# Kernel optimization log

Hardware: AMD Instinct MI355X
Metric: run time of the kernel (lower is better)

## Reference

```python
import jax, jax.numpy as jnp
import numpy as np

B, L, D, H, V = 4, 2048, 512, 8, 50257
NCAND, K, MAXM, NL, DFF = 64, 5, 10, 2, 4 * 512
HD = D // H


def _ln(x, g, b, eps=1e-5):
    m = jnp.mean(x, -1, keepdims=True)
    v = jnp.mean((x - m) ** 2, -1, keepdims=True)
    return (x - m) * jax.lax.rsqrt(v + eps) * g + b


def _mha(x, in_w, in_b, out_w, out_b):
    Bx, Lx, Dx = x.shape
    qkv = x @ in_w.T + in_b                      # [B,L,3D]
    q, k, v = jnp.split(qkv, 3, axis=-1)
    heads = lambda t: t.reshape(Bx, Lx, H, HD).transpose(0, 2, 1, 3)  # [B,H,L,hd]
    q, k, v = heads(q), heads(k), heads(v)
    s = jnp.einsum('bhqd,bhkd->bhqk', q, k) * np.float32(1.0 / np.sqrt(HD))
    a = jax.nn.softmax(s, axis=-1)
    o = jnp.einsum('bhqk,bhkd->bhqd', a, v).transpose(0, 2, 1, 3).reshape(Bx, Lx, Dx)
    return o @ out_w.T + out_b


def _encoder(x, p):
    # torch TransformerEncoderLayer default: post-LN, ReLU, dropout off (eval)
    for i in range(NL):
        x = _ln(x + _mha(x, p['attn_in_w'][i], p['attn_in_b'][i], p['attn_out_w'][i], p['attn_out_b'][i]), p['ln1_g'][i], p['ln1_b'][i])
        h = jax.nn.relu(x @ p['ffn_w1'][i].T + p['ffn_b1'][i]) @ p['ffn_w2'][i].T + p['ffn_b2'][i]
        x = _ln(x + h, p['ln2_g'][i], p['ln2_b'][i])
    return x


def _forward(token_ids, candidate_embeds, p):
    x = p['tok_emb'][token_ids] + p['pos_emb'][jnp.arange(L)][None]
    hidden = _encoder(x, p)                                  # [B,L,D]
    start_logits = hidden @ p['start_w'] + p['start_b']      # [B,L]
    end_logits = hidden @ p['end_w'] + p['end_b']
    s_idx = jax.lax.top_k(start_logits, K)[1]                # [B,K]
    e_idx = jax.lax.top_k(end_logits, K)[1]
    valid = (e_idx >= s_idx) & ((e_idx - s_idx) < MAXM)      # span validity mask
    h_s = jnp.take_along_axis(hidden, s_idx[..., None], axis=1)  # [B,K,D]
    h_e = jnp.take_along_axis(hidden, e_idx[..., None], axis=1)
    feat = jnp.concatenate([h_s, h_e, h_s * h_e], axis=-1)   # [B,K,3D]
    span = jax.nn.relu(feat @ p['span_w1'].T + p['span_b1']) @ p['span_w2'].T + p['span_b2']
    # compact valid spans to the front (ragged-to-padded), pad rest with zeros
    order = jnp.argsort((~valid).astype(jnp.int32), axis=1)  # stable: valid first
    span = jnp.take_along_axis(span, order[..., None], axis=1)
    vs = jnp.take_along_axis(valid, order, axis=1)
    span = span * vs[..., None].astype(span.dtype)           # [B,K,D]
    mp = span @ p['mention_w'].T + p['mention_b']
    cp = candidate_embeds @ p['entity_w'].T + p['entity_b']
    scores = jnp.einsum('bmd,bmcd->bmc', mp, cp)             # [B,K,NCAND]
    return span, start_logits, end_logits, hidden, scores


PARAM_KEYS = ['tok_emb', 'pos_emb', 'attn_in_w', 'attn_in_b', 'attn_out_w', 'attn_out_b',
              'ln1_g', 'ln1_b', 'ffn_w1', 'ffn_b1', 'ffn_w2', 'ffn_b2', 'ln2_g', 'ln2_b',
              'start_w', 'start_b', 'end_w', 'end_b', 'span_w1', 'span_b1', 'span_w2', 'span_b2',
              'mention_w', 'mention_b', 'entity_w', 'entity_b']


def setup_inputs() -> dict:
    key = jax.random.key(0)
    ks = iter(jax.random.split(key, 32))
    n = lambda shape, s=0.02: jax.random.normal(next(ks), shape, jnp.float32) * s
    return {
        'token_ids': jax.random.randint(next(ks), (B, L), 0, V),
        'candidate_embeds': jax.random.normal(next(ks), (B, K, NCAND, D), jnp.float32),
        'tok_emb': n((V, D)), 'pos_emb': n((L, D)),
        'attn_in_w': n((NL, 3 * D, D)), 'attn_in_b': n((NL, 3 * D)),
        'attn_out_w': n((NL, D, D)), 'attn_out_b': n((NL, D)),
        'ln1_g': jnp.ones((NL, D)), 'ln1_b': jnp.zeros((NL, D)),
        'ffn_w1': n((NL, DFF, D)), 'ffn_b1': n((NL, DFF)),
        'ffn_w2': n((NL, D, DFF)), 'ffn_b2': n((NL, D)),
        'ln2_g': jnp.ones((NL, D)), 'ln2_b': jnp.zeros((NL, D)),
        'start_w': n((D,)), 'start_b': jnp.zeros(()),
        'end_w': n((D,)), 'end_b': jnp.zeros(()),
        'span_w1': n((D, 3 * D)), 'span_b1': jnp.zeros((D,)),
        'span_w2': n((D, D)), 'span_b2': jnp.zeros((D,)),
        'mention_w': n((D, D)), 'mention_b': jnp.zeros((D,)),
        'entity_w': n((D, D)), 'entity_b': jnp.zeros((D,)),
    }


def reference(token_ids, candidate_embeds, tok_emb, pos_emb, attn_in_w, attn_in_b, attn_out_w, attn_out_b,
              ln1_g, ln1_b, ffn_w1, ffn_b1, ffn_w2, ffn_b2, ln2_g, ln2_b,
              start_w, start_b, end_w, end_b, span_w1, span_b1, span_w2, span_b2,
              mention_w, mention_b, entity_w, entity_b):
    loc = locals()
    p = {k: loc[k] for k in PARAM_KEYS}
    return _forward(token_ids, candidate_embeds, p)
```

## Files before the change

### kernel.cpp

```cpp
#include <hip/hip_runtime.h>
#include <hip/hip_bf16.h>
#include <cstddef>

#define BQ 4
#define LQ 2048
#define DQ 512
#define HQ 8
#define HDQ 64
#define KQ 5
#define MAXMQ 10

typedef __attribute__((ext_vector_type(8))) __bf16 bf16x8;
typedef __attribute__((ext_vector_type(4))) __bf16 bf16x4;
typedef __attribute__((ext_vector_type(4))) float f32x4;

__device__ inline void gload_lds16(const void* g, void* l) {
  __builtin_amdgcn_global_load_lds(
      (const __attribute__((address_space(1))) unsigned*)g,
      (__attribute__((address_space(3))) unsigned*)l, 16, 0, 0);
}

__device__ inline unsigned pack_bf16(float a, float b) {
  unsigned short ua = __builtin_bit_cast(unsigned short, (__bf16)a);
  unsigned short ub = __builtin_bit_cast(unsigned short, (__bf16)b);
  return (unsigned)ua | ((unsigned)ub << 16);
}

__device__ inline unsigned pack2(__bf16 a, __bf16 b) {
  return (unsigned)__builtin_bit_cast(unsigned short, a) |
         ((unsigned)__builtin_bit_cast(unsigned short, b) << 16);
}

__device__ inline float bf_lo(unsigned u) {
  return (float)__builtin_bit_cast(__bf16, (unsigned short)(u & 0xffff));
}
__device__ inline float bf_hi(unsigned u) {
  return (float)__builtin_bit_cast(__bf16, (unsigned short)(u >> 16));
}

__global__ __launch_bounds__(256) void prep_kernel(
    const float* __restrict__ s0, const float* __restrict__ s1,
    const float* __restrict__ s2, const float* __restrict__ s3,
    __bf16* __restrict__ d0, __bf16* __restrict__ d1,
    __bf16* __restrict__ d2, __bf16* __restrict__ d3,
    const float* __restrict__ ew_in, float* __restrict__ ew_out,
    const int* __restrict__ tok, const float* __restrict__ te,
    const float* __restrict__ pe, __bf16* __restrict__ xb) {
  __shared__ float t[32][33];
  const int bid = blockIdx.x;
  if (bid < 3072) {
    size_t g = ((size_t)bid * 256 + threadIdx.x) * 8;
    const float* src; __bf16* dst; size_t e;
    if (g < 1572864)      { src = s0; dst = d0; e = g; }
    else if (g < 2097152) { src = s1; dst = d1; e = g - 1572864; }
    else if (g < 4194304) { src = s2; dst = d2; e = g - 2097152; }
    else                  { src = s3; dst = d3; e = g - 4194304; }
    float4 a = *(const float4*)(src + e);
    float4 b = *(const float4*)(src + e + 4);
    bf16x8 v;
    v[0] = (__bf16)a.x; v[1] = (__bf16)a.y; v[2] = (__bf16)a.z; v[3] = (__bf16)a.w;
    v[4] = (__bf16)b.x; v[5] = (__bf16)b.y; v[6] = (__bf16)b.z; v[7] = (__bf16)b.w;
    *(bf16x8*)(dst + e) = v;
  } else if (bid < 3328) {
    int blk = bid - 3072;
    int bx = blk & 15, by = blk >> 4;
    int cx = threadIdx.x & 31, ry = threadIdx.x >> 5;
    #pragma unroll
    for (int i = 0; i < 4; ++i)
      t[ry + i * 8][cx] = ew_in[(size_t)(by * 32 + ry + i * 8) * 512 + bx * 32 + cx];
    __syncthreads();
    #pragma unroll
    for (int i = 0; i < 4; ++i)
      ew_out[(size_t)(bx * 32 + ry + i * 8) * 512 + by * 32 + cx] = t[cx][ry + i * 8];
  } else {
    int row = bid - 3328;
    int l = row & (LQ - 1);
    int tk = tok[row];
    int d = 2 * threadIdx.x;
    float2 tv = *(const float2*)&te[(size_t)tk * DQ + d];
    float2 pv = *(const float2*)&pe[(size_t)l * DQ + d];
    *(unsigned*)&xb[(size_t)row * DQ + d] = pack_bf16(tv.x + pv.x, tv.y + pv.y);
  }
}

template<int BN, bool RELU, bool HASRES>
__global__ __launch_bounds__(256) void bgemm_kernel(
    const __bf16* __restrict__ A, const __bf16* __restrict__ W,
    const float* __restrict__ bias, const __bf16* __restrict__ R,
    __bf16* __restrict__ Cb, int M, int N, int K) {
  __shared__ __bf16 As[2][128][32];
  __shared__ __bf16 Bs[2][BN][32];
  constexpr int NF = BN / 32;
  const int tid = threadIdx.x;
  const int w = tid >> 6, lane = tid & 63;
  const int lr = lane & 15, lg = lane >> 4;
  const int wr = w >> 1, wc = w & 1;
  const int m0 = blockIdx.y * 128, n0 = blockIdx.x * BN;

  f32x4 acc[4][NF];
  #pragma unroll
  for (int m = 0; m < 4; ++m)
    #pragma unroll
    for (int n = 0; n < NF; ++n) acc[m][n] = f32x4{0.f, 0.f, 0.f, 0.f};

  const int srowA = w * 32 + (lane >> 2);
  const int scol = (lane & 3) * 8;
  const int srowB = (BN == 128) ? srowA : (w * 16 + (lane >> 2));
  const __bf16* Ag = A + (size_t)(m0 + srowA) * K + scol;
  const __bf16* Bg = W + (size_t)(n0 + srowB) * K + scol;

  const int NT = K / 32;

  auto stage = [&](int t, int buf) {
    const int k1 = t * 32;
    gload_lds16(Ag + k1, &As[buf][w * 32][0]);
    gload_lds16(Ag + 16 * K + k1, &As[buf][w * 32 + 16][0]);
    if (BN == 128) {
      gload_lds16(Bg + k1, &Bs[buf][(w * 32) % BN][0]);
      gload_lds16(Bg + 16 * K + k1, &Bs[buf][(w * 32 + 16) % BN][0]);
    } else {
      gload_lds16(Bg + k1, &Bs[buf][(w * 16) % BN][0]);
    }
  };

  auto step = [&](int t, int cur) {
    __syncthreads();
    if (t + 1 < NT) stage(t + 1, cur ^ 1);
    bf16x8 af[4], bfr[NF];
    #pragma unroll
    for (int m = 0; m < 4; ++m) af[m] = *(bf16x8*)&As[cur][wr * 64 + m * 16 + lr][lg * 8];
    #pragma unroll
    for (int n = 0; n < NF; ++n) bfr[n] = *(bf16x8*)&Bs[cur][wc * (BN / 2) + n * 16 + lr][lg * 8];
    __builtin_amdgcn_s_setprio(1);
    #pragma unroll
    for (int m = 0; m < 4; ++m)
      #pragma unroll
      for (int n = 0; n < NF; ++n)
        acc[m][n] = __builtin_amdgcn_mfma_f32_16x16x32_bf16(af[m], bfr[n], acc[m][n], 0, 0, 0);
    __builtin_amdgcn_s_setprio(0);
  };

  stage(0, 0);
  for (int t = 0; t < NT; t += 2) { step(t, 0); step(t + 1, 1); }

  const int crow = m0 + wr * 64 + lg * 4;
  const int ccol = n0 + wc * (BN / 2) + lr;
  #pragma unroll
  for (int n = 0; n < NF; ++n) {
    int gc = ccol + n * 16;
    float bn = bias ? bias[gc] : 0.f;
    #pragma unroll
    for (int m = 0; m < 4; ++m) {
      #pragma unroll
      for (int reg = 0; reg < 4; ++reg) {
        int gr = crow + m * 16 + reg;
        float v = acc[m][n][reg] + bn;
        if (HASRES) v += (float)R[(size_t)gr * N + gc];
        if (RELU) v = fmaxf(v, 0.f);
        Cb[(size_t)gr * N + gc] = (__bf16)v;
      }
    }
  }
}

template<int MR, bool RELU, bool MASK>
__global__ __launch_bounds__(256) void tinygemm_kernel(
    const float* __restrict__ A, const float* __restrict__ W,
    const float* __restrict__ bias, const int* __restrict__ vs,
    float* __restrict__ C, int N, int K) {
  int n = blockIdx.x * 4 + (threadIdx.x >> 6);
  int lane = threadIdx.x & 63;
  if (n >= N) return;
  const float* wr = W + (size_t)n * K;
  float acc[MR];
  #pragma unroll
  for (int m = 0; m < MR; ++m) acc[m] = 0.f;
  for (int k = lane; k < K; k += 64) {
    float wv = wr[k];
    #pragma unroll
    for (int m = 0; m < MR; ++m)
      acc[m] += A[(size_t)m * K + k] * wv;
  }
  #pragma unroll
  for (int m = 0; m < MR; ++m) {
    #pragma unroll
    for (int off = 32; off; off >>= 1) acc[m] += __shfl_xor(acc[m], off);
  }
  if (lane == 0) {
    float bn = bias ? bias[n] : 0.f;
    #pragma unroll
    for (int m = 0; m < MR; ++m) {
      float v = acc[m] + bn;
      if (RELU) v = fmaxf(v, 0.f);
      if (MASK) v *= (float)vs[m];
      C[(size_t)m * N + n] = v;
    }
  }
}

__global__ __launch_bounds__(512) void attn_mfma_kernel(const __bf16* __restrict__ qkv,
                                                        __bf16* __restrict__ ob) {
  __shared__ __bf16 Ks[2][4096];
  __shared__ __bf16 Vt[2][64][72];
  __shared__ __bf16 Ps[8][1024];

  const int tid = threadIdx.x;
  const int wave = tid >> 6;
  const int lane = tid & 63;
  const int lr = lane & 15;
  const int lg = lane >> 4;

  const int bid = blockIdx.x;
  const int swz = (bid & 7) * 64 + (bid >> 3);
  const int bh = swz >> 4;
  const int qb = swz & 15;
  const int b = bh >> 3, h = bh & 7;
  const int q0 = qb * 128 + wave * 16;

  const __bf16* base = qkv + (size_t)b * LQ * 1536;

  bf16x8 aq[2];
  {
    const __bf16* qp = base + (size_t)(q0 + lr) * 1536 + h * 64 + lg * 8;
    aq[0] = *(const bf16x8*)qp;
    aq[1] = *(const bf16x8*)(qp + 32);
  }

  const int krow = tid >> 3;
  const int kdc = (tid & 7) ^ (krow & 7);
  const __bf16* gK = base + (size_t)krow * 1536 + 512 + h * 64 + kdc * 8;

  const int pr2 = tid >> 4;
  const int dq = tid & 15;
  const int vd0 = dq * 4;
  const __bf16* gV = base + (size_t)(2 * pr2) * 1536 + 1024 + h * 64 + vd0;
  const int pc2 = 2 * (pr2 & 3) + 8 * ((pr2 >> 2) ^ (dq >> 1));

  const int STEP = 64 * 1536;

  float lsum = 0.f;
  f32x4 o_acc[4];
  #pragma unroll
  for (int df = 0; df < 4; ++df) o_acc[df] = f32x4{0.f, 0.f, 0.f, 0.f};

  const float KE = 0.125f * 1.44269504f;

  gload_lds16(gK, &Ks[0][64 * wave * 8]);
  {
    bf16x4 v0 = *(const bf16x4*)gV;
    bf16x4 v1 = *(const bf16x4*)(gV + 1536);
    #pragma unroll
    for (int i = 0; i < 4; ++i)
      *(unsigned*)&Vt[0][vd0 + i][pc2] = pack2(v0[i], v1[i]);
  }
  gK += STEP; gV += STEP;

  auto tile = [&](int cur, bool more) {
    __syncthreads();
    bf16x4 nv0, nv1;
    if (more) {
      gload_lds16(gK, &Ks[cur ^ 1][64 * wave * 8]);
      nv0 = *(const bf16x4*)gV;
      nv1 = *(const bf16x4*)(gV + 1536);
      gK += STEP; gV += STEP;
    }

    f32x4 s[4];
    __builtin_amdgcn_s_setprio(1);
    #pragma unroll
    for (int f = 0; f < 4; ++f) {
      f32x4 acc = f32x4{0.f, 0.f, 0.f, 0.f};
      #pragma unroll
      for (int c = 0; c < 2; ++c) {
        bf16x8 ak = *(bf16x8*)&Ks[cur][(f * 16 + lr) * 64 + (((4 * c + lg) ^ (lr & 7)) << 3)];
        acc = __builtin_amdgcn_mfma_f32_16x16x32_bf16(ak, aq[c], acc, 0, 0, 0);
      }
      s[f] = acc;
    }
    __builtin_amdgcn_s_setprio(0);

    float rs = 0.f;
    #pragma unroll
    for (int f = 0; f < 4; ++f)
      #pragma unroll
      for (int r = 0; r < 4; ++r) {
        float p = exp2f(s[f][r] * KE);
        s[f][r] = p;
        rs += p;
      }
    rs += __shfl_xor(rs, 16);
    rs += __shfl_xor(rs, 32);
    lsum += rs;

    #pragma unroll
    for (int f = 0; f < 4; ++f) {
      uint2 pv;
      pv.x = pack_bf16(s[f][0], s[f][1]);
      pv.y = pack_bf16(s[f][2], s[f][3]);
      int chunk = 2 * f + (lg >> 1);
      int eoff = ((chunk ^ (lr & 7)) << 3) + ((lg & 1) << 2);
      *(uint2*)&Ps[wave][lr * 64 + eoff] = pv;
    }

    #pragma unroll
    for (int kc = 0; kc < 2; ++kc) {
      bf16x8 bp = *(bf16x8*)&Ps[wave][lr * 64 + (((4 * kc + lg) ^ (lr & 7)) << 3)];
      __builtin_amdgcn_s_setprio(1);
      #pragma unroll
      for (int df = 0; df < 4; ++df) {
        int vrow = df * 16 + lr;
        int pb = (((4 * kc + lg) ^ ((vrow >> 3) & 7)) << 3);
        bf16x8 av = *(bf16x8*)&Vt[cur][vrow][pb];
        o_acc[df] = __builtin_amdgcn_mfma_f32_16x16x32_bf16(av, bp, o_acc[df], 0, 0, 0);
      }
      __builtin_amdgcn_s_setprio(0);
    }

    if (more) {
      #pragma unroll
      for (int i = 0; i < 4; ++i)
        *(unsigned*)&Vt[cur ^ 1][vd0 + i][pc2] = pack2(nv0[i], nv1[i]);
    }
  };

  for (int kt = 0; kt < LQ / 64; kt += 2) {
    tile(0, true);
    tile(1, kt + 1 != LQ / 64 - 1);
  }

  float inv = 1.f / lsum;
  __bf16* orow = ob + ((size_t)(b * LQ) + q0 + lr) * DQ + h * 64 + lg * 4;
  #pragma unroll
  for (int df = 0; df < 4; ++df) {
    uint2 ov;
    ov.x = pack_bf16(o_acc[df][0] * inv, o_acc[df][1] * inv);
    ov.y = pack_bf16(o_acc[df][2] * inv, o_acc[df][3] * inv);
    *(uint2*)(orow + df * 16) = ov;
  }
}

template<bool WF32>
__global__ __launch_bounds__(256) void ln_kernel(const __bf16* __restrict__ t,
    const float* __restrict__ g, const float* __restrict__ bb,
    __bf16* __restrict__ xb, float* __restrict__ xf) {
  int row = blockIdx.x;
  int tid = threadIdx.x;
  unsigned u = *(const unsigned*)&t[(size_t)row * DQ + 2 * tid];
  float v0 = bf_lo(u), v1 = bf_hi(u);
  float s = v0 + v1, ss = v0 * v0 + v1 * v1;
  #pragma unroll
  for (int off = 32; off; off >>= 1) { s += __shfl_xor(s, off); ss += __shfl_xor(ss, off); }
  __shared__ float rs[4], rss[4];
  int w = tid >> 6;
  if ((tid & 63) == 0) { rs[w] = s; rss[w] = ss; }
  __syncthreads();
  s = rs[0] + rs[1] + rs[2] + rs[3];
  ss = rss[0] + rss[1] + rss[2] + rss[3];
  float mean = s * (1.f / 512.f);
  float var = ss * (1.f / 512.f) - mean * mean;
  float r = rsqrtf(var + 1e-5f);
  float2 gg = *(const float2*)&g[2 * tid];
  float2 bv = *(const float2*)&bb[2 * tid];
  float o0 = (v0 - mean) * r * gg.x + bv.x;
  float o1 = (v1 - mean) * r * gg.y + bv.y;
  *(unsigned*)&xb[(size_t)row * DQ + 2 * tid] = pack_bf16(o0, o1);
  if (WF32) {
    float2 of; of.x = o0; of.y = o1;
    *(float2*)&xf[(size_t)row * DQ + 2 * tid] = of;
  }
}

__global__ __launch_bounds__(256) void logits_kernel(const float* __restrict__ hidden,
    const float* __restrict__ sw, const float* __restrict__ sb,
    const float* __restrict__ ew, const float* __restrict__ eb,
    float* __restrict__ osl, float* __restrict__ oel) {
  int row = blockIdx.x * 4 + (threadIdx.x >> 6);
  int lane = threadIdx.x & 63;
  const float* hr = hidden + (size_t)row * DQ;
  float a = 0.f, b2 = 0.f;
  #pragma unroll
  for (int i = 0; i < 8; ++i) {
    int d = lane + i * 64;
    float h = hr[d];
    a += h * sw[d];
    b2 += h * ew[d];
  }
  #pragma unroll
  for (int off = 32; off; off >>= 1) { a += __shfl_xor(a, off); b2 += __shfl_xor(b2, off); }
  if (lane == 0) { osl[row] = a + sb[0]; oel[row] = b2 + eb[0]; }
}

__global__ void topk_kernel(const float* __restrict__ slog, const float* __restrict__ elog,
                            int* __restrict__ sidx, int* __restrict__ eidx) {
  int b = blockIdx.x & 3;
  int which = blockIdx.x >> 2;
  const float* lg = (which ? elog : slog) + (size_t)b * LQ;
  int* outp = (which ? eidx : sidx) + b * KQ;
  int lane = threadIdx.x;
  int ch[KQ];
  for (int k = 0; k < KQ; ++k) {
    float bv = -1e38f; int bi = 1 << 30;
    for (int i = lane; i < LQ; i += 64) {
      bool skip = false;
      for (int t = 0; t < k; ++t) if (ch[t] == i) skip = true;
      float v = lg[i];
      if (!skip && (v > bv || (v == bv && i < bi))) { bv = v; bi = i; }
    }
    #pragma unroll
    for (int off = 32; off; off >>= 1) {
      float ov = __shfl_xor(bv, off); int oi = __shfl_xor(bi, off);
      if (ov > bv || (ov == bv && oi < bi)) { bv = ov; bi = oi; }
    }
    ch[k] = bi;
    if (lane == 0) outp[k] = bi;
  }
}

__global__ void vo_kernel(const int* __restrict__ sidx, const int* __restrict__ eidx,
                          int* __restrict__ order, int* __restrict__ vs) {
  int b = threadIdx.x;
  if (b >= BQ) return;
  int val[KQ];
  for (int k = 0; k < KQ; ++k) {
    int s = sidx[b * KQ + k], e = eidx[b * KQ + k];
    val[k] = (e >= s && (e - s) < MAXMQ) ? 1 : 0;
  }
  int j = 0;
  for (int k = 0; k < KQ; ++k) if (val[k])  { order[b * KQ + j] = k; vs[b * KQ + j] = 1; ++j; }
  for (int k = 0; k < KQ; ++k) if (!val[k]) { order[b * KQ + j] = k; vs[b * KQ + j] = 0; ++j; }
}

__global__ __launch_bounds__(256) void feat_kernel(const float* __restrict__ hidden,
    const int* __restrict__ sidx, const int* __restrict__ eidx,
    const int* __restrict__ order, float* __restrict__ feat) {
  int row = blockIdx.x;
  int b = row / KQ;
  int k = order[row];
  int si = sidx[b * KQ + k], ei = eidx[b * KQ + k];
  const float* hs = hidden + ((size_t)(b * LQ + si)) * DQ;
  const float* he = hidden + ((size_t)(b * LQ + ei)) * DQ;
  float* fr = feat + (size_t)row * (3 * DQ);
  for (int d = threadIdx.x; d < DQ; d += 256) {
    float a = hs[d], c = he[d];
    fr[d] = a; fr[DQ + d] = c; fr[2 * DQ + d] = a * c;
  }
}

__global__ __launch_bounds__(256) void scores_kernel(const float* __restrict__ cand,
    const float* __restrict__ mp, const float* __restrict__ u, const float* __restrict__ ebias,
    float* __restrict__ oscores) {
  int gw = blockIdx.x * 4 + (threadIdx.x >> 6);
  int lane = threadIdx.x & 63;
  int bj = gw >> 6;
  const float* ce = cand + (size_t)gw * DQ;
  const float* ur = u + (size_t)bj * DQ;
  const float* mr = mp + (size_t)bj * DQ;
  float s = 0.f;
  #pragma unroll
  for (int i = 0; i < 8; ++i) {
    int e = lane + i * 64;
    s += ce[e] * ur[e] + mr[e] * ebias[e];
  }
  #pragma unroll
  for (int off = 32; off; off >>= 1) s += __shfl_xor(s, off);
  if (lane == 0) oscores[gw] = s;
}

extern "C" void kernel_launch(void* const* d_in, const int* in_sizes, int n_in,
                              void* d_out, int out_size, void* d_ws, size_t ws_size,
                              hipStream_t stream) {
  const int*   token_ids = (const int*)d_in[0];
  const float* cand    = (const float*)d_in[1];
  const float* tok_emb = (const float*)d_in[2];
  const float* pos_emb = (const float*)d_in[3];
  const float* ain_w   = (const float*)d_in[4];
  const float* ain_b   = (const float*)d_in[5];
  const float* aout_w  = (const float*)d_in[6];
  const float* aout_b  = (const float*)d_in[7];
  const float* ln1g    = (const float*)d_in[8];
  const float* ln1b    = (const float*)d_in[9];
  const float* fw1     = (const float*)d_in[10];
  const float* fb1     = (const float*)d_in[11];
  const float* fw2     = (const float*)d_in[12];
  const float* fb2     = (const float*)d_in[13];
  const float* ln2g    = (const float*)d_in[14];
  const float* ln2b    = (const float*)d_in[15];
  const float* sw      = (const float*)d_in[16];
  const float* sb      = (const float*)d_in[17];
  const float* ew      = (const float*)d_in[18];
  const float* eb      = (const float*)d_in[19];
  const float* sp_w1   = (const float*)d_in[20];
  const float* sp_b1   = (const float*)d_in[21];
  const float* sp_w2   = (const float*)d_in[22];
  const float* sp_b2   = (const float*)d_in[23];
  const float* m_w     = (const float*)d_in[24];
  const float* m_b     = (const float*)d_in[25];
  const float* e_w     = (const float*)d_in[26];
  const float* e_b     = (const float*)d_in[27];

  const int M = BQ * LQ;
  float* out = (float*)d_out;
  float* out_span   = out;
  float* out_sl     = out + 10240;
  float* out_el     = out + 18432;
  float* out_hidden = out + 26624;
  float* out_scores = out + 4220928;

  float* ws  = (float*)d_ws;
  __bf16* BIGb = (__bf16*)ws;
  __bf16* Xb   = (__bf16*)(ws + 8388608);
  __bf16* Ob   = (__bf16*)(ws + 10485760);
  __bf16* Tb   = (__bf16*)(ws + 12582912);
  __bf16* ain_wb  = (__bf16*)(ws + 14680064);
  __bf16* aout_wb = (__bf16*)(ws + 15466496);
  __bf16* fw1b    = (__bf16*)(ws + 15728640);
  __bf16* fw2b    = (__bf16*)(ws + 16777216);
  float* e_wT     = ws + 17825792;
  int*   SIDX  = (int*)(ws + 18088064);
  int*   EIDX  = SIDX + 20;
  int*   ORDER = EIDX + 20;
  int*   VS    = ORDER + 20;
  float* FEAT    = ws + 18088192;
  float* SPANH   = FEAT + 30720;
  float* MP      = SPANH + 10240;
  float* U       = MP + 10240;

  prep_kernel<<<11520, 256, 0, stream>>>(ain_w, aout_w, fw1, fw2,
                                         ain_wb, aout_wb, fw1b, fw2b,
                                         e_w, e_wT, token_ids, tok_emb, pos_emb, Xb);

  for (int l = 0; l < 2; ++l) {
    bgemm_kernel<128, false, false><<<dim3(12, 64), 256, 0, stream>>>(
        Xb, ain_wb + (size_t)l * 1536 * 512, ain_b + l * 1536, nullptr,
        BIGb, M, 1536, 512);
    attn_mfma_kernel<<<512, 512, 0, stream>>>(BIGb, Ob);
    bgemm_kernel<128, false, true><<<dim3(4, 64), 256, 0, stream>>>(
        Ob, aout_wb + (size_t)l * 512 * 512, aout_b + l * 512, Xb,
        Tb, M, 512, 512);
    ln_kernel<false><<<M, 256, 0, stream>>>(Tb, ln1g + l * 512, ln1b + l * 512,
                                            Xb, nullptr);
    bgemm_kernel<128, true, false><<<dim3(16, 64), 256, 0, stream>>>(
        Xb, fw1b + (size_t)l * 2048 * 512, fb1 + l * 2048, nullptr,
        BIGb, M, 2048, 512);
    bgemm_kernel<128, false, true><<<dim3(4, 64), 256, 0, stream>>>(
        BIGb, fw2b + (size_t)l * 512 * 2048, fb2 + l * 512, Xb,
        Tb, M, 512, 2048);
    if (l == 0)
      ln_kernel<false><<<M, 256, 0, stream>>>(Tb, ln2g, ln2b, Xb, nullptr);
    else
      ln_kernel<true><<<M, 256, 0, stream>>>(Tb, ln2g + 512, ln2b + 512,
                                             Xb, out_hidden);
  }

  logits_kernel<<<M / 4, 256, 0, stream>>>(out_hidden, sw, sb, ew, eb, out_sl, out_el);
  topk_kernel<<<8, 64, 0, stream>>>(out_sl, out_el, SIDX, EIDX);
  vo_kernel<<<1, 64, 0, stream>>>(SIDX, EIDX, ORDER, VS);
  feat_kernel<<<20, 256, 0, stream>>>(out_hidden, SIDX, EIDX, ORDER, FEAT);
  tinygemm_kernel<20, true, false><<<128, 256, 0, stream>>>(
      FEAT, sp_w1, sp_b1, nullptr, SPANH, 512, 1536);
  tinygemm_kernel<20, false, true><<<128, 256, 0, stream>>>(
      SPANH, sp_w2, sp_b2, VS, out_span, 512, 512);
  tinygemm_kernel<20, false, false><<<128, 256, 0, stream>>>(
      out_span, m_w, m_b, nullptr, MP, 512, 512);
  tinygemm_kernel<20, false, false><<<128, 256, 0, stream>>>(
      MP, e_wT, nullptr, nullptr, U, 512, 512);
  scores_kernel<<<320, 256, 0, stream>>>(cand, MP, U, e_b, out_scores);
}
```

Before: 487.2 us.

## Split-K the N=512 GEMMs and fuse bias, residual and LayerNorm into the reduce

The out-projection and FFN2 GEMMs (N=512, only 256 blocks) now use a 2-way split-K kernel that writes fp32 partials. A new LN kernel sums the partials and adds bias and residual before normalizing. On the final layer it also computes the start/end logits, which removes a separate logits pass. topk and the validity/order kernels are merged into one launch, and the attention kernel gets an occupancy hint in its launch bounds. Doubling the block count improves CU fill, at the cost of extra fp32 partial traffic (two 8192x512 fp32 buffers) and a larger workspace.

Result: slower. 500.9 us (+2.8%).

```diff
diff --git a/kernel.cpp b/kernel.cpp
--- a/kernel.cpp
+++ b/kernel.cpp
@@ -83,31 +83,29 @@
   }
 }
 
-template<int BN, bool RELU, bool HASRES>
+template<bool RELU>
 __global__ __launch_bounds__(256) void bgemm_kernel(
     const __bf16* __restrict__ A, const __bf16* __restrict__ W,
-    const float* __restrict__ bias, const __bf16* __restrict__ R,
-    __bf16* __restrict__ Cb, int M, int N, int K) {
+    const float* __restrict__ bias, __bf16* __restrict__ Cb,
+    int M, int N, int K) {
   __shared__ __bf16 As[2][128][32];
-  __shared__ __bf16 Bs[2][BN][32];
-  constexpr int NF = BN / 32;
+  __shared__ __bf16 Bs[2][128][32];
   const int tid = threadIdx.x;
   const int w = tid >> 6, lane = tid & 63;
   const int lr = lane & 15, lg = lane >> 4;
   const int wr = w >> 1, wc = w & 1;
-  const int m0 = blockIdx.y * 128, n0 = blockIdx.x * BN;
-
-  f32x4 acc[4][NF];
+  const int m0 = blockIdx.y * 128, n0 = blockIdx.x * 128;
+
+  f32x4 acc[4][4];
   #pragma unroll
   for (int m = 0; m < 4; ++m)
     #pragma unroll
-    for (int n = 0; n < NF; ++n) acc[m][n] = f32x4{0.f, 0.f, 0.f, 0.f};
-
-  const int srowA = w * 32 + (lane >> 2);
+    for (int n = 0; n < 4; ++n) acc[m][n] = f32x4{0.f, 0.f, 0.f, 0.f};
+
+  const int srow = w * 32 + (lane >> 2);
   const int scol = (lane & 3) * 8;
-  const int srowB = (BN == 128) ? srowA : (w * 16 + (lane >> 2));
-  const __bf16* Ag = A + (size_t)(m0 + srowA) * K + scol;
-  const __bf16* Bg = W + (size_t)(n0 + srowB) * K + scol;
+  const __bf16* Ag = A + (size_t)(m0 + srow) * K + scol;
+  const __bf16* Bg = W + (size_t)(n0 + srow) * K + scol;
 
   const int NT = K / 32;
 
@@ -115,27 +113,23 @@
     const int k1 = t * 32;
     gload_lds16(Ag + k1, &As[buf][w * 32][0]);
     gload_lds16(Ag + 16 * K + k1, &As[buf][w * 32 + 16][0]);
-    if (BN == 128) {
-      gload_lds16(Bg + k1, &Bs[buf][(w * 32) % BN][0]);
-      gload_lds16(Bg + 16 * K + k1, &Bs[buf][(w * 32 + 16) % BN][0]);
-    } else {
-      gload_lds16(Bg + k1, &Bs[buf][(w * 16) % BN][0]);
-    }
+    gload_lds16(Bg + k1, &Bs[buf][w * 32][0]);
+    gload_lds16(Bg + 16 * K + k1, &Bs[buf][w * 32 + 16][0]);
   };
 
   auto step = [&](int t, int cur) {
     __syncthreads();
     if (t + 1 < NT) stage(t + 1, cur ^ 1);
-    bf16x8 af[4], bfr[NF];
+    bf16x8 af[4], bfr[4];
     #pragma unroll
     for (int m = 0; m < 4; ++m) af[m] = *(bf16x8*)&As[cur][wr * 64 + m * 16 + lr][lg * 8];
     #pragma unroll
-    for (int n = 0; n < NF; ++n) bfr[n] = *(bf16x8*)&Bs[cur][wc * (BN / 2) + n * 16 + lr][lg * 8];
+    for (int n = 0; n < 4; ++n) bfr[n] = *(bf16x8*)&Bs[cur][wc * 64 + n * 16 + lr][lg * 8];
     __builtin_amdgcn_s_setprio(1);
     #pragma unroll
     for (int m = 0; m < 4; ++m)
       #pragma unroll
-      for (int n = 0; n < NF; ++n)
+      for (int n = 0; n < 4; ++n)
         acc[m][n] = __builtin_amdgcn_mfma_f32_16x16x32_bf16(af[m], bfr[n], acc[m][n], 0, 0, 0);
     __builtin_amdgcn_s_setprio(0);
   };
@@ -144,21 +138,141 @@
   for (int t = 0; t < NT; t += 2) { step(t, 0); step(t + 1, 1); }
 
   const int crow = m0 + wr * 64 + lg * 4;
-  const int ccol = n0 + wc * (BN / 2) + lr;
-  #pragma unroll
-  for (int n = 0; n < NF; ++n) {
+  const int ccol = n0 + wc * 64 + lr;
+  #pragma unroll
+  for (int n = 0; n < 4; ++n) {
     int gc = ccol + n * 16;
-    float bn = bias ? bias[gc] : 0.f;
+    float bn = bias[gc];
     #pragma unroll
     for (int m = 0; m < 4; ++m) {
       #pragma unroll
       for (int reg = 0; reg < 4; ++reg) {
         int gr = crow + m * 16 + reg;
         float v = acc[m][n][reg] + bn;
-        if (HASRES) v += (float)R[(size_t)gr * N + gc];
         if (RELU) v = fmaxf(v, 0.f);
         Cb[(size_t)gr * N + gc] = (__bf16)v;
       }
+    }
+  }
+}
+
+__global__ __launch_bounds__(256) void bgemm_sk_kernel(
+    const __bf16* __restrict__ A, const __bf16* __restrict__ W,
+    float* __restrict__ P, int M, int N, int K) {
+  __shared__ __bf16 As[2][128][32];
+  __shared__ __bf16 Bs[2][128][32];
+  const int tid = threadIdx.x;
+  const int w = tid >> 6, lane = tid & 63;
+  const int lr = lane & 15, lg = lane >> 4;
+  const int wr = w >> 1, wc = w & 1;
+  const int m0 = blockIdx.y * 128, n0 = blockIdx.x * 128;
+  const int ks = blockIdx.z;
+  const int kh = K / 2;
+
+  f32x4 acc[4][4];
+  #pragma unroll
+  for (int m = 0; m < 4; ++m)
+    #pragma unroll
+    for (int n = 0; n < 4; ++n) acc[m][n] = f32x4{0.f, 0.f, 0.f, 0.f};
+
+  const int srow = w * 32 + (lane >> 2);
+  const int scol = (lane & 3) * 8;
+  const __bf16* Ag = A + (size_t)(m0 + srow) * K + ks * kh + scol;
+  const __bf16* Bg = W + (size_t)(n0 + srow) * K + ks * kh + scol;
+
+  const int NT = kh / 32;
+
+  auto stage = [&](int t, int buf) {
+    const int k1 = t * 32;
+    gload_lds16(Ag + k1, &As[buf][w * 32][0]);
+    gload_lds16(Ag + 16 * K + k1, &As[buf][w * 32 + 16][0]);
+    gload_lds16(Bg + k1, &Bs[buf][w * 32][0]);
+    gload_lds16(Bg + 16 * K + k1, &Bs[buf][w * 32 + 16][0]);
+  };
+
+  auto step = [&](int t, int cur) {
+    __syncthreads();
+    if (t + 1 < NT) stage(t + 1, cur ^ 1);
+    bf16x8 af[4], bfr[4];
+    #pragma unroll
+    for (int m = 0; m < 4; ++m) af[m] = *(bf16x8*)&As[cur][wr * 64 + m * 16 + lr][lg * 8];
+    #pragma unroll
+    for (int n = 0; n < 4; ++n) bfr[n] = *(bf16x8*)&Bs[cur][wc * 64 + n * 16 + lr][lg * 8];
+    __builtin_amdgcn_s_setprio(1);
+    #pragma unroll
+    for (int m = 0; m < 4; ++m)
+      #pragma unroll
+      for (int n = 0; n < 4; ++n)
+        acc[m][n] = __builtin_amdgcn_mfma_f32_16x16x32_bf16(af[m], bfr[n], acc[m][n], 0, 0, 0);
+    __builtin_amdgcn_s_setprio(0);
+  };
+
+  stage(0, 0);
+  for (int t = 0; t < NT; t += 2) { step(t, 0); step(t + 1, 1); }
+
+  float* Pk = P + (size_t)ks * M * N;
+  const int crow = m0 + wr * 64 + lg * 4;
+  const int ccol = n0 + wc * 64 + lr;
+  #pragma unroll
+  for (int n = 0; n < 4; ++n) {
+    int gc = ccol + n * 16;
+    #pragma unroll
+    for (int m = 0; m < 4; ++m)
+      #pragma unroll
+      for (int reg = 0; reg < 4; ++reg)
+        Pk[(size_t)(crow + m * 16 + reg) * N + gc] = acc[m][n][reg];
+  }
+}
+
+template<bool FIN>
+__global__ __launch_bounds__(256) void lnc_kernel(
+    const float* __restrict__ P, const float* __restrict__ bias,
+    __bf16* __restrict__ Xb, const float* __restrict__ g,
+    const float* __restrict__ bb, float* __restrict__ xf,
+    const float* __restrict__ sw, const float* __restrict__ sb,
+    const float* __restrict__ ew, const float* __restrict__ eb,
+    float* __restrict__ osl, float* __restrict__ oel) {
+  int row = blockIdx.x;
+  int tid = threadIdx.x;
+  int d = 2 * tid;
+  float2 p0 = *(const float2*)&P[(size_t)row * DQ + d];
+  float2 p1 = *(const float2*)&P[(size_t)(BQ * LQ) * DQ + (size_t)row * DQ + d];
+  float2 bi = *(const float2*)&bias[d];
+  unsigned ur = *(const unsigned*)&Xb[(size_t)row * DQ + d];
+  float v0 = p0.x + p1.x + bi.x + bf_lo(ur);
+  float v1 = p0.y + p1.y + bi.y + bf_hi(ur);
+  float s = v0 + v1, ss = v0 * v0 + v1 * v1;
+  #pragma unroll
+  for (int off = 32; off; off >>= 1) { s += __shfl_xor(s, off); ss += __shfl_xor(ss, off); }
+  __shared__ float rs[4], rss[4];
+  int w = tid >> 6;
+  if ((tid & 63) == 0) { rs[w] = s; rss[w] = ss; }
+  __syncthreads();
+  s = rs[0] + rs[1] + rs[2] + rs[3];
+  ss = rss[0] + rss[1] + rss[2] + rss[3];
+  float mean = s * (1.f / 512.f);
+  float var = ss * (1.f / 512.f) - mean * mean;
+  float r = rsqrtf(var + 1e-5f);
+  float2 gg = *(const float2*)&g[d];
+  float2 bv = *(const float2*)&bb[d];
+  float o0 = (v0 - mean) * r * gg.x + bv.x;
+  float o1 = (v1 - mean) * r * gg.y + bv.y;
+  *(unsigned*)&Xb[(size_t)row * DQ + d] = pack_bf16(o0, o1);
+  if (FIN) {
+    float2 of; of.x = o0; of.y = o1;
+    *(float2*)&xf[(size_t)row * DQ + d] = of;
+    float2 swv = *(const float2*)&sw[d];
+    float2 ewv = *(const float2*)&ew[d];
+    float a = o0 * swv.x + o1 * swv.y;
+    float b2 = o0 * ewv.x + o1 * ewv.y;
+    #pragma unroll
+    for (int off = 32; off; off >>= 1) { a += __shfl_xor(a, off); b2 += __shfl_xor(b2, off); }
+    __shared__ float ra[4], rb[4];
+    if ((tid & 63) == 0) { ra[w] = a; rb[w] = b2; }
+    __syncthreads();
+    if (tid == 0) {
+      osl[row] = ra[0] + ra[1] + ra[2] + ra[3] + sb[0];
+      oel[row] = rb[0] + rb[1] + rb[2] + rb[3] + eb[0];
     }
   }
 }
@@ -198,8 +312,8 @@
   }
 }
 
-__global__ __launch_bounds__(512) void attn_mfma_kernel(const __bf16* __restrict__ qkv,
-                                                        __bf16* __restrict__ ob) {
+__global__ __launch_bounds__(512, 6) void attn_mfma_kernel(const __bf16* __restrict__ qkv,
+                                                           __bf16* __restrict__ ob) {
   __shared__ __bf16 Ks[2][4096];
   __shared__ __bf16 Vt[2][64][72];
   __shared__ __bf16 Ps[8][1024];
@@ -339,10 +453,9 @@
   }
 }
 
-template<bool WF32>
 __global__ __launch_bounds__(256) void ln_kernel(const __bf16* __restrict__ t,
     const float* __restrict__ g, const float* __restrict__ bb,
-    __bf16* __restrict__ xb, float* __restrict__ xf) {
+    __bf16* __restrict__ xb) {
   int row = blockIdx.x;
   int tid = threadIdx.x;
   unsigned u = *(const unsigned*)&t[(size_t)row * DQ + 2 * tid];
@@ -364,39 +477,17 @@
   float o0 = (v0 - mean) * r * gg.x + bv.x;
   float o1 = (v1 - mean) * r * gg.y + bv.y;
   *(unsigned*)&xb[(size_t)row * DQ + 2 * tid] = pack_bf16(o0, o1);
-  if (WF32) {
-    float2 of; of.x = o0; of.y = o1;
-    *(float2*)&xf[(size_t)row * DQ + 2 * tid] = of;
-  }
-}
-
-__global__ __launch_bounds__(256) void logits_kernel(const float* __restrict__ hidden,
-    const float* __restrict__ sw, const float* __restrict__ sb,
-    const float* __restrict__ ew, const float* __restrict__ eb,
-    float* __restrict__ osl, float* __restrict__ oel) {
-  int row = blockIdx.x * 4 + (threadIdx.x >> 6);
+}
+
+__global__ void topkvo_kernel(const float* __restrict__ slog, const float* __restrict__ elog,
+                              int* __restrict__ sidx, int* __restrict__ eidx,
+                              int* __restrict__ order, int* __restrict__ vs) {
+  int b = blockIdx.x;
+  int which = threadIdx.x >> 6;
   int lane = threadIdx.x & 63;
-  const float* hr = hidden + (size_t)row * DQ;
-  float a = 0.f, b2 = 0.f;
-  #pragma unroll
-  for (int i = 0; i < 8; ++i) {
-    int d = lane + i * 64;
-    float h = hr[d];
-    a += h * sw[d];
-    b2 += h * ew[d];
-  }
-  #pragma unroll
-  for (int off = 32; off; off >>= 1) { a += __shfl_xor(a, off); b2 += __shfl_xor(b2, off); }
-  if (lane == 0) { osl[row] = a + sb[0]; oel[row] = b2 + eb[0]; }
-}
-
-__global__ void topk_kernel(const float* __restrict__ slog, const float* __restrict__ elog,
-                            int* __restrict__ sidx, int* __restrict__ eidx) {
-  int b = blockIdx.x & 3;
-  int which = blockIdx.x >> 2;
   const float* lg = (which ? elog : slog) + (size_t)b * LQ;
   int* outp = (which ? eidx : sidx) + b * KQ;
-  int lane = threadIdx.x;
+  __shared__ int sel[2][KQ];
   int ch[KQ];
   for (int k = 0; k < KQ; ++k) {
     float bv = -1e38f; int bi = 1 << 30;
@@ -412,22 +503,19 @@
       if (ov > bv || (ov == bv && oi < bi)) { bv = ov; bi = oi; }
     }
     ch[k] = bi;
-    if (lane == 0) outp[k] = bi;
-  }
-}
-
-__global__ void vo_kernel(const int* __restrict__ sidx, const int* __restrict__ eidx,
-                          int* __restrict__ order, int* __restrict__ vs) {
-  int b = threadIdx.x;
-  if (b >= BQ) return;
-  int val[KQ];
-  for (int k = 0; k < KQ; ++k) {
-    int s = sidx[b * KQ + k], e = eidx[b * KQ + k];
-    val[k] = (e >= s && (e - s) < MAXMQ) ? 1 : 0;
-  }
-  int j = 0;
-  for (int k = 0; k < KQ; ++k) if (val[k])  { order[b * KQ + j] = k; vs[b * KQ + j] = 1; ++j; }
-  for (int k = 0; k < KQ; ++k) if (!val[k]) { order[b * KQ + j] = k; vs[b * KQ + j] = 0; ++j; }
+    if (lane == 0) { outp[k] = bi; sel[which][k] = bi; }
+  }
+  __syncthreads();
+  if (threadIdx.x == 0) {
+    int val[KQ];
+    for (int k = 0; k < KQ; ++k) {
+      int s = sel[0][k], e = sel[1][k];
+      val[k] = (e >= s && (e - s) < MAXMQ) ? 1 : 0;
+    }
+    int j = 0;
+    for (int k = 0; k < KQ; ++k) if (val[k])  { order[b * KQ + j] = k; vs[b * KQ + j] = 1; ++j; }
+    for (int k = 0; k < KQ; ++k) if (!val[k]) { order[b * KQ + j] = k; vs[b * KQ + j] = 0; ++j; }
+  }
 }
 
 __global__ __launch_bounds__(256) void feat_kernel(const float* __restrict__ hidden,
@@ -510,17 +598,17 @@
   __bf16* BIGb = (__bf16*)ws;
   __bf16* Xb   = (__bf16*)(ws + 8388608);
   __bf16* Ob   = (__bf16*)(ws + 10485760);
-  __bf16* Tb   = (__bf16*)(ws + 12582912);
-  __bf16* ain_wb  = (__bf16*)(ws + 14680064);
-  __bf16* aout_wb = (__bf16*)(ws + 15466496);
-  __bf16* fw1b    = (__bf16*)(ws + 15728640);
-  __bf16* fw2b    = (__bf16*)(ws + 16777216);
-  float* e_wT     = ws + 17825792;
-  int*   SIDX  = (int*)(ws + 18088064);
+  float*  Pbuf = ws + 12582912;
+  __bf16* ain_wb  = (__bf16*)(ws + 20971520);
+  __bf16* aout_wb = (__bf16*)(ws + 21757952);
+  __bf16* fw1b    = (__bf16*)(ws + 22020096);
+  __bf16* fw2b    = (__bf16*)(ws + 23068672);
+  float* e_wT     = ws + 24117248;
+  int*   SIDX  = (int*)(ws + 24379392);
   int*   EIDX  = SIDX + 20;
   int*   ORDER = EIDX + 20;
   int*   VS    = ORDER + 20;
-  float* FEAT    = ws + 18088192;
+  float* FEAT    = ws + 24379520;
   float* SPANH   = FEAT + 30720;
   float* MP      = SPANH + 10240;
   float* U       = MP + 10240;
@@ -530,31 +618,29 @@
                                          e_w, e_wT, token_ids, tok_emb, pos_emb, Xb);
 
   for (int l = 0; l < 2; ++l) {
-    bgemm_kernel<128, false, false><<<dim3(12, 64), 256, 0, stream>>>(
-        Xb, ain_wb + (size_t)l * 1536 * 512, ain_b + l * 1536, nullptr,
-        BIGb, M, 1536, 512);
+    bgemm_kernel<false><<<dim3(12, 64), 256, 0, stream>>>(
+        Xb, ain_wb + (size_t)l * 1536 * 512, ain_b + l * 1536, BIGb, M, 1536, 512);
     attn_mfma_kernel<<<512, 512, 0, stream>>>(BIGb, Ob);
-    bgemm_kernel<128, false, true><<<dim3(4, 64), 256, 0, stream>>>(
-        Ob, aout_wb + (size_t)l * 512 * 512, aout_b + l * 512, Xb,
-        Tb, M, 512, 512);
-    ln_kernel<false><<<M, 256, 0, stream>>>(Tb, ln1g + l * 512, ln1b + l * 512,
-                                            Xb, nullptr);
-    bgemm_kernel<128, true, false><<<dim3(16, 64), 256, 0, stream>>>(
-        Xb, fw1b + (size_t)l * 2048 * 512, fb1 + l * 2048, nullptr,
-        BIGb, M, 2048, 512);
-    bgemm_kernel<128, false, true><<<dim3(4, 64), 256, 0, stream>>>(
-        BIGb, fw2b + (size_t)l * 512 * 2048, fb2 + l * 512, Xb,
-        Tb, M, 512, 2048);
+    bgemm_sk_kernel<<<dim3(4, 64, 2), 256, 0, stream>>>(
+        Ob, aout_wb + (size_t)l * 512 * 512, Pbuf, M, 512, 512);
+    lnc_kernel<false><<<M, 256, 0, stream>>>(
+        Pbuf, aout_b + l * 512, Xb, ln1g + l * 512, ln1b + l * 512,
+        nullptr, nullptr, nullptr, nullptr, nullptr, nullptr, nullptr);
+    bgemm_kernel<true><<<dim3(16, 64), 256, 0, stream>>>(
+        Xb, fw1b + (size_t)l * 2048 * 512, fb1 + l * 2048, BIGb, M, 2048, 512);
+    bgemm_sk_kernel<<<dim3(4, 64, 2), 256, 0, stream>>>(
+        BIGb, fw2b + (size_t)l * 512 * 2048, Pbuf, M, 512, 2048);
     if (l == 0)
-      ln_kernel<false><<<M, 256, 0, stream>>>(Tb, ln2g, ln2b, Xb, nullptr);
+      lnc_kernel<false><<<M, 256, 0, stream>>>(
+          Pbuf, fb2, Xb, ln2g, ln2b,
+          nullptr, nullptr, nullptr, nullptr, nullptr, nullptr, nullptr);
     else
-      ln_kernel<true><<<M, 256, 0, stream>>>(Tb, ln2g + 512, ln2b + 512,
-                                             Xb, out_hidden);
-  }
-
-  logits_kernel<<<M / 4, 256, 0, stream>>>(out_hidden, sw, sb, ew, eb, out_sl, out_el);
-  topk_kernel<<<8, 64, 0, stream>>>(out_sl, out_el, SIDX, EIDX);
-  vo_kernel<<<1, 64, 0, stream>>>(SIDX, EIDX, ORDER, VS);
+      lnc_kernel<true><<<M, 256, 0, stream>>>(
+          Pbuf, fb2 + 512, Xb, ln2g + 512, ln2b + 512,
+          out_hidden, sw, sb, ew, eb, out_sl, out_el);
+  }
+
+  topkvo_kernel<<<4, 128, 0, stream>>>(out_sl, out_el, SIDX, EIDX, ORDER, VS);
   feat_kernel<<<20, 256, 0, stream>>>(out_hidden, SIDX, EIDX, ORDER, FEAT);
   tinygemm_kernel<20, true, false><<<128, 256, 0, stream>>>(
       FEAT, sp_w1, sp_b1, nullptr, SPANH, 512, 1536);
```
